# Kernel tuning notes

Measured on AMD Instinct MI355X. Metric: run time of the kernel, lower is better.

## Reference

```python
import jax, jax.numpy as jnp
import numpy as np

BS, NE, NN, CIN, H, D = 8, 4800, 4981, 3, 128, 6
EPG = 19200
NEDGE = BS * EPG
N = BS * NE

PARAM_NAMES = [
    'enc_cw1','enc_cb1','enc_cw2','enc_cb2','enc_cw3','enc_clng','enc_clnb',
    'enc_ew1','enc_eb1','enc_ew2','enc_eb2','enc_ew3','enc_elng','enc_elnb',
    'p_ew1','p_eb1','p_ew2','p_eb2','p_ew3','p_elng','p_elnb',
    'p_nw1','p_nb1','p_nw2','p_nb2','p_nw3','p_nlng','p_nlnb',
    'dec_uw1','dec_ub1','dec_uw2','dec_ub2','dec_uw3','dec_ulng','dec_ulnb',
    'dec_cw1','dec_cb1','dec_cw2','dec_cb2','dec_cw3']


def setup_inputs():
    key = jax.random.key(0)
    ks = iter(jax.random.split(key, 64))
    def nrm(shape, s=0.1):
        return jax.random.normal(next(ks), shape, jnp.float32) * s
    inp = {}
    inp['x'] = jax.random.normal(next(ks), (BS * NN, CIN), jnp.float32)
    inp['elem_conn'] = jax.random.randint(next(ks), (NE, 4), 0, NN)
    inp['edge_index'] = jax.random.randint(next(ks), (2, NEDGE), 0, N)
    inp['enc_cw1'] = nrm((CIN, 4, 1)); inp['enc_cb1'] = nrm((CIN, 1), 0.01)
    inp['enc_cw2'] = nrm((CIN, 1, 1)); inp['enc_cb2'] = nrm((CIN, 1), 0.01)
    inp['enc_cw3'] = nrm((CIN, 1, 1))
    inp['enc_clng'] = jnp.ones((CIN, 1)); inp['enc_clnb'] = jnp.zeros((CIN, 1))
    inp['enc_ew1'] = nrm((CIN, H)); inp['enc_eb1'] = nrm((H,), 0.01)
    inp['enc_ew2'] = nrm((H, H)); inp['enc_eb2'] = nrm((H,), 0.01)
    inp['enc_ew3'] = nrm((H, H))
    inp['enc_elng'] = jnp.ones((H,)); inp['enc_elnb'] = jnp.zeros((H,))
    inp['p_ew1'] = nrm((D, 2 * H, H)); inp['p_eb1'] = nrm((D, H), 0.01)
    inp['p_ew2'] = nrm((D, H, H)); inp['p_eb2'] = nrm((D, H), 0.01)
    inp['p_ew3'] = nrm((D, H, H))
    inp['p_elng'] = jnp.ones((D, H)); inp['p_elnb'] = jnp.zeros((D, H))
    inp['p_nw1'] = nrm((D, 2 * H, H)); inp['p_nb1'] = nrm((D, H), 0.01)
    inp['p_nw2'] = nrm((D, H, H)); inp['p_nb2'] = nrm((D, H), 0.01)
    inp['p_nw3'] = nrm((D, H, H))
    inp['p_nlng'] = jnp.ones((D, H)); inp['p_nlnb'] = jnp.zeros((D, H))
    inp['dec_uw1'] = nrm((H, 1, 4)); inp['dec_ub1'] = nrm((H, 4), 0.01)
    inp['dec_uw2'] = nrm((H, 4, 4)); inp['dec_ub2'] = nrm((H, 4), 0.01)
    inp['dec_uw3'] = nrm((H, 4, 4))
    inp['dec_ulng'] = jnp.ones((H, 4)); inp['dec_ulnb'] = jnp.zeros((H, 4))
    inp['dec_cw1'] = nrm((H, CIN)); inp['dec_cb1'] = nrm((CIN,), 0.01)
    inp['dec_cw2'] = nrm((CIN, CIN)); inp['dec_cb2'] = nrm((CIN,), 0.01)
    inp['dec_cw3'] = nrm((CIN, CIN))
    return inp


def lrelu(x):
    return jnp.where(x >= 0, x, 0.2 * x)


def ln(x, g, b, axis=-1):
    m = jnp.mean(x, axis=axis, keepdims=True)
    v = jnp.var(x, axis=axis, keepdims=True)
    return (x - m) / jnp.sqrt(v + 1e-5) * g + b


def mlp(x, w1, b1, w2, b2, w3):
    h = lrelu(x @ w1 + b1)
    h = lrelu(h @ w2 + b2)
    return h @ w3


def _forward(fl, elem_conn, edge_index):
    x = fl[0]
    P = dict(zip(PARAM_NAMES, fl[1:]))
    # ---- Encoder: MeshCNN gather (4 mesh nodes per element) + per-channel MLP 4->1 ----
    xg = x.reshape(BS, NN, CIN)[:, elem_conn]                  # (BS, NE, 4, CIN)
    h = lrelu(jnp.einsum('beic,cio->beoc', xg, P['enc_cw1']) + P['enc_cb1'].T[None, None])
    h = lrelu(jnp.einsum('beic,cio->beoc', h, P['enc_cw2']) + P['enc_cb2'].T[None, None])
    h = jnp.einsum('beic,cio->beoc', h, P['enc_cw3'])
    h = ln(h, P['enc_clng'].T[None, None], P['enc_clnb'].T[None, None], axis=2)  # LayerNorm(1)
    h = h[:, :, 0, :].reshape(N, CIN)
    h = ln(mlp(h, P['enc_ew1'], P['enc_eb1'], P['enc_ew2'], P['enc_eb2'], P['enc_ew3']),
           P['enc_elng'], P['enc_elnb'])                       # (N, H)
    # ---- Processor: D GraphNet blocks, edge MLP + scatter-add + node MLP ----
    src, dest = edge_index[0], edge_index[1]
    stacked = (P['p_ew1'], P['p_eb1'], P['p_ew2'], P['p_eb2'], P['p_ew3'], P['p_elng'], P['p_elnb'],
               P['p_nw1'], P['p_nb1'], P['p_nw2'], P['p_nb2'], P['p_nw3'], P['p_nlng'], P['p_nlnb'])
    def step(hc, p):
        ew1, eb1, ew2, eb2, ew3, eg, ebv, nw1, nb1, nw2, nb2, nw3, ng, nbv = p
        msg = jnp.concatenate([hc[dest], hc[src]], axis=-1)    # (NEDGE, 2H)
        m = ln(mlp(msg, ew1, eb1, ew2, eb2, ew3), eg, ebv)
        aggr = jax.ops.segment_sum(m, dest, num_segments=N)
        hn = ln(mlp(jnp.concatenate([hc, aggr], axis=-1), nw1, nb1, nw2, nb2, nw3), ng, nbv)
        return hn, None
    h, _ = jax.lax.scan(step, h, stacked)
    # ---- Decoder: per-channel upsample 1->4 then index_add back to mesh nodes ----
    u = h.reshape(BS, NE, H)[:, :, None, :]                    # (BS, NE, 1, H)
    u = lrelu(jnp.einsum('beic,cio->beoc', u, P['dec_uw1']) + P['dec_ub1'].T[None, None])
    u = lrelu(jnp.einsum('beic,cio->beoc', u, P['dec_uw2']) + P['dec_ub2'].T[None, None])
    u = jnp.einsum('beic,cio->beoc', u, P['dec_uw3'])
    u = ln(u, P['dec_ulng'].T[None, None], P['dec_ulnb'].T[None, None], axis=2)  # (BS, NE, 4, H)
    out = jnp.zeros((BS, NN, H), u.dtype).at[:, elem_conn.reshape(-1)].add(u.reshape(BS, NE * 4, H))
    out = out.reshape(BS * NN, H)
    o = lrelu(out @ P['dec_cw1'] + P['dec_cb1'])
    o = lrelu(o @ P['dec_cw2'] + P['dec_cb2'])
    return o @ P['dec_cw3']


def reference(x, elem_conn, edge_index,
              enc_cw1, enc_cb1, enc_cw2, enc_cb2, enc_cw3, enc_clng, enc_clnb,
              enc_ew1, enc_eb1, enc_ew2, enc_eb2, enc_ew3, enc_elng, enc_elnb,
              p_ew1, p_eb1, p_ew2, p_eb2, p_ew3, p_elng, p_elnb,
              p_nw1, p_nb1, p_nw2, p_nb2, p_nw3, p_nlng, p_nlnb,
              dec_uw1, dec_ub1, dec_uw2, dec_ub2, dec_uw3, dec_ulng, dec_ulnb,
              dec_cw1, dec_cb1, dec_cw2, dec_cb2, dec_cw3):
    fl = (x, enc_cw1, enc_cb1, enc_cw2, enc_cb2, enc_cw3, enc_clng, enc_clnb,
          enc_ew1, enc_eb1, enc_ew2, enc_eb2, enc_ew3, enc_elng, enc_elnb,
          p_ew1, p_eb1, p_ew2, p_eb2, p_ew3, p_elng, p_elnb,
          p_nw1, p_nb1, p_nw2, p_nb2, p_nw3, p_nlng, p_nlnb,
          dec_uw1, dec_ub1, dec_uw2, dec_ub2, dec_uw3, dec_ulng, dec_ulnb,
          dec_cw1, dec_cb1, dec_cw2, dec_cb2, dec_cw3)
    return _forward(fl, elem_conn, edge_index)
```

## Files before the change

### kernel.cpp

```cpp
#include <hip/hip_runtime.h>
#include <hip/hip_fp16.h>
#include <math.h>

#define BS    8
#define NE    4800
#define NN    4981
#define CIN   3
#define HD    128
#define DBLK  6
#define NEDGE 153600
#define NTOT  38400
#define NMESH (BS*NN)
#define NNP   5120
#define EM    128
#define NTILE (NEDGE / EM)
#define EGRID 240
#define TPB   (NTILE / EGRID)

#define UW1T  0
#define UB1T  512
#define UW2T  1024
#define UB2T  3072
#define UW3T  3584
#define ULNGT 5632
#define ULNBT 6144
#define DWT_N 6656

typedef _Float16 f16;
typedef _Float16 f16x8 __attribute__((ext_vector_type(8)));
typedef float f32x4 __attribute__((ext_vector_type(4)));

__device__ __forceinline__ float lrelu(float x) { return x >= 0.0f ? x : 0.2f * x; }

__global__ __launch_bounds__(128)
void enc_const_kernel(const float* __restrict__ clnb,
                      const float* __restrict__ ew1, const float* __restrict__ eb1,
                      const float* __restrict__ ew2, const float* __restrict__ eb2,
                      const float* __restrict__ ew3,
                      const float* __restrict__ g, const float* __restrict__ b,
                      float* __restrict__ hv0) {
    __shared__ float s1[HD], s2[HD], s3[HD];
    int j = threadIdx.x;
    float a = eb1[j];
    for (int c = 0; c < CIN; ++c) a += clnb[c] * ew1[c * HD + j];
    s1[j] = lrelu(a);
    __syncthreads();
    a = eb2[j];
    for (int k = 0; k < HD; ++k) a += s1[k] * ew2[k * HD + j];
    s2[j] = lrelu(a);
    __syncthreads();
    a = 0.0f;
    for (int k = 0; k < HD; ++k) a += s2[k] * ew3[k * HD + j];
    s3[j] = a;
    __syncthreads();
    float m = 0.0f;
    for (int k = 0; k < HD; ++k) m += s3[k];
    m *= (1.0f / HD);
    float v = 0.0f;
    for (int k = 0; k < HD; ++k) { float d = s3[k] - m; v += d * d; }
    v *= (1.0f / HD);
    float rs = 1.0f / sqrtf(v + 1e-5f);
    hv0[j] = (s3[j] - m) * rs * g[j] + b[j];
}

__global__ __launch_bounds__(128)
void msg0_kernel(const float* __restrict__ hv0,
                 const float* __restrict__ ew1, const float* __restrict__ eb1,
                 const float* __restrict__ ew2, const float* __restrict__ eb2,
                 const float* __restrict__ ew3,
                 const float* __restrict__ g, const float* __restrict__ b,
                 float* __restrict__ m0) {
    __shared__ float s1[HD], s2[HD], s3[HD];
    int j = threadIdx.x;
    float a = eb1[j];
    for (int k = 0; k < HD; ++k) a += hv0[k] * (ew1[k * HD + j] + ew1[(k + HD) * HD + j]);
    s1[j] = lrelu(a);
    __syncthreads();
    a = eb2[j];
    for (int k = 0; k < HD; ++k) a += s1[k] * ew2[k * HD + j];
    s2[j] = lrelu(a);
    __syncthreads();
    a = 0.0f;
    for (int k = 0; k < HD; ++k) a += s2[k] * ew3[k * HD + j];
    s3[j] = a;
    __syncthreads();
    float m = 0.0f;
    for (int k = 0; k < HD; ++k) m += s3[k];
    m *= (1.0f / HD);
    float v = 0.0f;
    for (int k = 0; k < HD; ++k) { float d = s3[k] - m; v += d * d; }
    v *= (1.0f / HD);
    float rs = 1.0f / sqrtf(v + 1e-5f);
    m0[j] = (s3[j] - m) * rs * g[j] + b[j];
}

__global__ __launch_bounds__(256)
void init_h16_kernel(f16* __restrict__ h, const float* __restrict__ hv0, int n8) {
    __shared__ f16 v[HD];
    if (threadIdx.x < HD) v[threadIdx.x] = (f16)hv0[threadIdx.x];
    __syncthreads();
    for (int i = blockIdx.x * blockDim.x + threadIdx.x; i < n8; i += gridDim.x * blockDim.x)
        ((uint4*)h)[i] = ((const uint4*)v)[i & 15];
}

__global__ __launch_bounds__(256)
void conv_weights_kernel(const float* __restrict__ ew1, const float* __restrict__ ew2,
                         const float* __restrict__ ew3,
                         const float* __restrict__ nw1, const float* __restrict__ nw2,
                         const float* __restrict__ nw3, f16* __restrict__ wbuf) {
    int b = blockIdx.x;
    int d = b >> 3, m = b & 7;
    const float* src;
    switch (m) {
        case 0: src = ew1 + (size_t)d * 2 * HD * HD; break;
        case 1: src = ew1 + (size_t)d * 2 * HD * HD + HD * HD; break;
        case 2: src = ew2 + (size_t)d * HD * HD; break;
        case 3: src = ew3 + (size_t)d * HD * HD; break;
        case 4: src = nw1 + (size_t)d * 2 * HD * HD; break;
        case 5: src = nw1 + (size_t)d * 2 * HD * HD + HD * HD; break;
        case 6: src = nw2 + (size_t)d * HD * HD; break;
        default: src = nw3 + (size_t)d * HD * HD; break;
    }
    f16* out = wbuf + (size_t)b * HD * HD;
    for (int idx = threadIdx.x; idx < HD * HD; idx += 256) {
        int n = idx >> 7, k = idx & 127;
        out[idx] = (f16)src[k * HD + n];
    }
}

__global__ __launch_bounds__(256)
void conv_ebias_kernel(const float* __restrict__ eb1, f16* __restrict__ eb16) {
    for (int i = threadIdx.x; i < DBLK * HD; i += 256)
        eb16[i] = (f16)eb1[i];
}

__global__ __launch_bounds__(256)
void conv_dec_weights(const float* __restrict__ uw1, const float* __restrict__ ub1,
                      const float* __restrict__ uw2, const float* __restrict__ ub2,
                      const float* __restrict__ uw3, const float* __restrict__ ulng,
                      const float* __restrict__ ulnb, float* __restrict__ dwt) {
    int tid = threadIdx.x;
    for (int idx = tid; idx < 512; idx += 256) {
        int o = idx >> 7, c = idx & 127;
        dwt[UW1T + idx] = uw1[c * 4 + o];
        dwt[UB1T + idx] = ub1[c * 4 + o];
        dwt[UB2T + idx] = ub2[c * 4 + o];
        dwt[ULNGT + idx] = ulng[c * 4 + o];
        dwt[ULNBT + idx] = ulnb[c * 4 + o];
    }
    for (int idx = tid; idx < 2048; idx += 256) {
        int io = idx >> 7, c = idx & 127;
        dwt[UW2T + idx] = uw2[c * 16 + io];
        dwt[UW3T + idx] = uw3[c * 16 + io];
    }
}

__global__ __launch_bounds__(256)
void csr_hist(const int* __restrict__ key, int* __restrict__ deg, int n) {
    int e = blockIdx.x * 256 + threadIdx.x;
    if (e < n) atomicAdd(&deg[key[e]], 1);
}

__global__ __launch_bounds__(256)
void csr_scan1(const int* __restrict__ deg, int* __restrict__ rowptr,
               int* __restrict__ bsum) {
    __shared__ int s[256];
    int i = blockIdx.x * 256 + threadIdx.x;
    int v = deg[i];
    s[threadIdx.x] = v;
    __syncthreads();
    for (int off = 1; off < 256; off <<= 1) {
        int t = (threadIdx.x >= off) ? s[threadIdx.x - off] : 0;
        __syncthreads();
        s[threadIdx.x] += t;
        __syncthreads();
    }
    rowptr[i] = s[threadIdx.x] - v;
    if (threadIdx.x == 255) bsum[blockIdx.x] = s[255];
}

__global__ __launch_bounds__(256)
void csr_scan2(int* __restrict__ bsum, int nb) {
    __shared__ int s[256];
    int v = (threadIdx.x < nb) ? bsum[threadIdx.x] : 0;
    s[threadIdx.x] = v;
    __syncthreads();
    for (int off = 1; off < 256; off <<= 1) {
        int t = (threadIdx.x >= off) ? s[threadIdx.x - off] : 0;
        __syncthreads();
        s[threadIdx.x] += t;
        __syncthreads();
    }
    if (threadIdx.x < nb) bsum[threadIdx.x] = s[threadIdx.x] - v;
}

__global__ __launch_bounds__(256)
void csr_scan3(int* __restrict__ rowptr, const int* __restrict__ bsum) {
    int i = blockIdx.x * 256 + threadIdx.x;
    rowptr[i] += bsum[blockIdx.x];
}

__global__ __launch_bounds__(256)
void csr_scatter(const int* __restrict__ dest, const int* __restrict__ srcv,
                 const int* __restrict__ rowptr, int* __restrict__ cursor,
                 int* __restrict__ dsorted, int* __restrict__ ssorted) {
    int e = blockIdx.x * 256 + threadIdx.x;
    int d = dest[e];
    int pos = rowptr[d] + atomicAdd(&cursor[d], 1);
    dsorted[pos] = d;
    ssorted[pos] = srcv[e];
}

__global__ __launch_bounds__(256)
void mesh_scatter(const int* __restrict__ conn, const int* __restrict__ mrow,
                  int* __restrict__ mcur, int* __restrict__ mslot, int n) {
    int idx = blockIdx.x * 256 + threadIdx.x;
    if (idx < n) {
        int nd = conn[idx];
        int pos = mrow[nd] + atomicAdd(&mcur[nd], 1);
        mslot[pos] = idx;
    }
}

template <int NT>
__device__ __forceinline__ void stage_w(const f16* __restrict__ Wg, f16 (*Bt)[HD + 8],
                                        int tid) {
    #pragma unroll
    for (int t = 0; t < 2048 / NT; ++t) {
        int idx = tid + t * NT;
        int r = idx >> 4, c = (idx & 15) * 8;
        *(uint4*)(&Bt[r][c]) = *(const uint4*)(Wg + (size_t)r * HD + c);
    }
}

__device__ __forceinline__ void mfma_pass(const f16 (*A)[HD + 8], const f16 (*Bt)[HD + 8],
                                          int rt_base, int ct_base, int ln, int quad,
                                          f32x4 acc[2][4]) {
    #pragma unroll
    for (int ks = 0; ks < 4; ++ks) {
        int kb = ks * 32 + quad * 8;
        f16x8 a0 = *(const f16x8*)(&A[rt_base + ln][kb]);
        f16x8 a1 = *(const f16x8*)(&A[rt_base + 16 + ln][kb]);
        #pragma unroll
        for (int c = 0; c < 4; ++c) {
            f16x8 b = *(const f16x8*)(&Bt[ct_base + c * 16 + ln][kb]);
            acc[0][c] = __builtin_amdgcn_mfma_f32_16x16x32_f16(a0, b, acc[0][c], 0, 0, 0);
            acc[1][c] = __builtin_amdgcn_mfma_f32_16x16x32_f16(a1, b, acc[1][c], 0, 0, 0);
        }
    }
}

__global__ __launch_bounds__(512, 2)
void gn_edge(const f16* __restrict__ P1, const f16* __restrict__ P2,
             const int* __restrict__ dsorted, const int* __restrict__ ssorted,
             const f16* __restrict__ W2, const f16* __restrict__ W3,
             const f16* __restrict__ b1h, const float* __restrict__ b2,
             const float* __restrict__ g, const float* __restrict__ bln,
             f16* __restrict__ msg) {
    __shared__ __align__(16) f16 Ag[2][EM][HD + 8];
    __shared__ __align__(16) f16 Bt2[HD][HD + 8];
    __shared__ __align__(16) f16 Bt3[HD][HD + 8];
    __shared__ float red[EM][2][2];

    const int tid = threadIdx.x;
    const int wave = tid >> 6, lane = tid & 63;
    const int ln = lane & 15, quad = lane >> 4;
    const int rt_base = (wave >> 1) * 32;
    const int ct_base = (wave & 1) * 64;
    const int half = wave & 1;
    const int r0 = tid >> 4;
    const int cg = (tid & 15) * 8;

    const int t0 = blockIdx.x * TPB;
    const int t1 = t0 + TPB;

    const f16 k02s = (f16)0.2f;
    const f16x8 k02 = {k02s, k02s, k02s, k02s, k02s, k02s, k02s, k02s};
    const f16x8 bb = *(const f16x8*)(b1h + cg);

    int dI[4], sI[4];
    #pragma unroll
    for (int it = 0; it < 4; ++it) {
        dI[it] = dsorted[t0 * EM + r0 + it * 32];
        sI[it] = ssorted[t0 * EM + r0 + it * 32];
    }
    stage_w<512>(W2, Bt2, tid);
    stage_w<512>(W3, Bt3, tid);
    #pragma unroll
    for (int it = 0; it < 4; ++it) {
        f16x8 p1 = *(const f16x8*)(P1 + (size_t)dI[it] * HD + cg);
        f16x8 p2 = *(const f16x8*)(P2 + (size_t)sI[it] * HD + cg);
        f16x8 s = p1 + p2 + bb;
        *(f16x8*)(&Ag[0][r0 + it * 32][cg]) = __builtin_elementwise_max(s, s * k02);
    }
    #pragma unroll
    for (int it = 0; it < 4; ++it) {
        dI[it] = dsorted[(t0 + 1) * EM + r0 + it * 32];
        sI[it] = ssorted[(t0 + 1) * EM + r0 + it * 32];
    }
    __syncthreads();

    int b = 0;
    for (int t = t0; t < t1; ++t, b ^= 1) {
        const int base = t * EM;
        f32x4 acc[2][4];

        #pragma unroll
        for (int c = 0; c < 4; ++c) {
            float bj = b2[ct_base + c * 16 + ln];
            f32x4 bv = {bj, bj, bj, bj};
            acc[0][c] = bv; acc[1][c] = bv;
        }
        mfma_pass(Ag[b], Bt2, rt_base, ct_base, ln, quad, acc);
        __syncthreads();

        const bool hasNext = (t + 1 < t1);
        f16x8 q1[4], q2[4];
        if (hasNext) {
            #pragma unroll
            for (int it = 0; it < 4; ++it) {
                q1[it] = *(const f16x8*)(P1 + (size_t)dI[it] * HD + cg);
                q2[it] = *(const f16x8*)(P2 + (size_t)sI[it] * HD + cg);
            }
        }
        #pragma unroll
        for (int i = 0; i < 2; ++i)
            #pragma unroll
            for (int c = 0; c < 4; ++c)
                #pragma unroll
                for (int r = 0; r < 4; ++r)
                    Ag[b][rt_base + i * 16 + quad * 4 + r][ct_base + c * 16 + ln] =
                        (f16)lrelu(acc[i][c][r]);
        if (t + 2 < t1) {
            #pragma unroll
            for (int it = 0; it < 4; ++it) {
                dI[it] = dsorted[(t + 2) * EM + r0 + it * 32];
                sI[it] = ssorted[(t + 2) * EM + r0 + it * 32];
            }
        }
        __syncthreads();

        #pragma unroll
        for (int c = 0; c < 4; ++c) { f32x4 z = {0,0,0,0}; acc[0][c] = z; acc[1][c] = z; }
        mfma_pass(Ag[b], Bt3, rt_base, ct_base, ln, quad, acc);

        #pragma unroll
        for (int i = 0; i < 2; ++i)
            #pragma unroll
            for (int r = 0; r < 4; ++r) {
                float s = acc[i][0][r] + acc[i][1][r] + acc[i][2][r] + acc[i][3][r];
                float q = acc[i][0][r] * acc[i][0][r] + acc[i][1][r] * acc[i][1][r] +
                          acc[i][2][r] * acc[i][2][r] + acc[i][3][r] * acc[i][3][r];
                s += __shfl_xor(s, 1); q += __shfl_xor(q, 1);
                s += __shfl_xor(s, 2); q += __shfl_xor(q, 2);
                s += __shfl_xor(s, 4); q += __shfl_xor(q, 4);
                s += __shfl_xor(s, 8); q += __shfl_xor(q, 8);
                if (ln == 0) {
                    int row = rt_base + i * 16 + quad * 4 + r;
                    red[row][half][0] = s;
                    red[row][half][1] = q;
                }
            }

        if (hasNext) {
            #pragma unroll
            for (int it = 0; it < 4; ++it) {
                f16x8 s = q1[it] + q2[it] + bb;
                *(f16x8*)(&Ag[b ^ 1][r0 + it * 32][cg]) =
                    __builtin_elementwise_max(s, s * k02);
            }
        }
        __syncthreads();

        float gv[4], bv[4];
        #pragma unroll
        for (int c = 0; c < 4; ++c) {
            int col = ct_base + c * 16 + ln;
            gv[c] = g[col]; bv[c] = bln[col];
        }
        #pragma unroll
        for (int i = 0; i < 2; ++i)
            #pragma unroll
            for (int r = 0; r < 4; ++r) {
                int row = rt_base + i * 16 + quad * 4 + r;
                float s = red[row][0][0] + red[row][1][0];
                float q = red[row][0][1] + red[row][1][1];
                float m = s * (1.0f / HD);
                float var = q * (1.0f / HD) - m * m;
                float rs = 1.0f / sqrtf(var + 1e-5f);
                #pragma unroll
                for (int c = 0; c < 4; ++c) {
                    int col = ct_base + c * 16 + ln;
                    float v = (acc[i][c][r] - m) * rs * gv[c] + bv[c];
                    msg[(size_t)(base + row) * HD + col] = (f16)v;
                }
            }
    }
}

template <int AGGR, bool PROD>
__global__ __launch_bounds__(256, 3)
void gn_node(f16* __restrict__ h16, const f16* __restrict__ msg,
             const int* __restrict__ rowptr, const int* __restrict__ deg,
             const float* __restrict__ m0,
             const f16* __restrict__ W1a, const f16* __restrict__ W1b,
             const f16* __restrict__ W2, const f16* __restrict__ W3,
             const float* __restrict__ b1, const float* __restrict__ b2,
             const float* __restrict__ g, const float* __restrict__ bln,
             const f16* __restrict__ nW1a, const f16* __restrict__ nW1b,
             f16* __restrict__ P1, f16* __restrict__ P2) {
    __shared__ __align__(16) f16 As[64][HD + 8];
    __shared__ __align__(16) f16 Bt[HD][HD + 8];
    __shared__ float red[64][2][2];
    int* rpS = (int*)&red[0][0][0];
    int* dgS = rpS + 64;

    const int tid = threadIdx.x;
    const int base = blockIdx.x * 64;
    const int wave = tid >> 6, lane = tid & 63;
    const int ln = lane & 15, quad = lane >> 4;
    const int rt_base = (wave >> 1) * 32;
    const int ct_base = (wave & 1) * 64;
    const int half = wave & 1;

    if (tid < 64) {
        if (AGGR == 1) rpS[tid] = rowptr[base + tid];
        dgS[tid] = deg[base + tid];
    }
    __syncthreads();

    f16x8 hreg[4];
    #pragma unroll
    for (int t = 0; t < 4; ++t) {
        int idx = tid + t * 256;
        int r = idx >> 4, c = (idx & 15) * 8;
        hreg[t] = *(const f16x8*)(h16 + (size_t)(base + r) * HD + c);
        if (AGGR == 0) {
            float sc = (float)dgS[r];
            f16x8 o;
            #pragma unroll
            for (int u = 0; u < 8; ++u) o[u] = (f16)(sc * m0[c + u]);
            *(f16x8*)(&As[r][c]) = o;
        } else {
            int rp = rpS[r], dg = dgS[r];
            float a[8] = {0, 0, 0, 0, 0, 0, 0, 0};
            for (int j = 0; j < dg; ++j) {
                f16x8 mv = *(const f16x8*)(msg + (size_t)(rp + j) * HD + c);
                #pragma unroll
                for (int u = 0; u < 8; ++u) a[u] += (float)mv[u];
            }
            f16x8 o;
            #pragma unroll
            for (int u = 0; u < 8; ++u) o[u] = (f16)a[u];
            *(f16x8*)(&As[r][c]) = o;
        }
    }
    stage_w<256>(W1b, Bt, tid);
    __syncthreads();

    f32x4 acc[2][4];
    #pragma unroll
    for (int c = 0; c < 4; ++c) {
        float bj = b1[ct_base + c * 16 + ln];
        f32x4 bb = {bj, bj, bj, bj};
        acc[0][c] = bb; acc[1][c] = bb;
    }
    mfma_pass(As, Bt, rt_base, ct_base, ln, quad, acc);
    __syncthreads();

    #pragma unroll
    for (int t = 0; t < 4; ++t) {
        int idx = tid + t * 256;
        int r = idx >> 4, c = (idx & 15) * 8;
        *(f16x8*)(&As[r][c]) = hreg[t];
    }
    stage_w<256>(W1a, Bt, tid);
    __syncthreads();
    mfma_pass(As, Bt, rt_base, ct_base, ln, quad, acc);
    __syncthreads();

    stage_w<256>(W2, Bt, tid);
    #pragma unroll
    for (int i = 0; i < 2; ++i)
        #pragma unroll
        for (int c = 0; c < 4; ++c)
            #pragma unroll
            for (int r = 0; r < 4; ++r)
                As[rt_base + i * 16 + quad * 4 + r][ct_base + c * 16 + ln] =
                    (f16)lrelu(acc[i][c][r]);
    __syncthreads();

    #pragma unroll
    for (int c = 0; c < 4; ++c) {
        float bj = b2[ct_base + c * 16 + ln];
        f32x4 bb = {bj, bj, bj, bj};
        acc[0][c] = bb; acc[1][c] = bb;
    }
    mfma_pass(As, Bt, rt_base, ct_base, ln, quad, acc);
    __syncthreads();
    stage_w<256>(W3, Bt, tid);
    #pragma unroll
    for (int i = 0; i < 2; ++i)
        #pragma unroll
        for (int c = 0; c < 4; ++c)
            #pragma unroll
            for (int r = 0; r < 4; ++r)
                As[rt_base + i * 16 + quad * 4 + r][ct_base + c * 16 + ln] =
                    (f16)lrelu(acc[i][c][r]);
    __syncthreads();

    #pragma unroll
    for (int c = 0; c < 4; ++c) { f32x4 z = {0,0,0,0}; acc[0][c] = z; acc[1][c] = z; }
    mfma_pass(As, Bt, rt_base, ct_base, ln, quad, acc);

    #pragma unroll
    for (int i = 0; i < 2; ++i)
        #pragma unroll
        for (int r = 0; r < 4; ++r) {
            float s = acc[i][0][r] + acc[i][1][r] + acc[i][2][r] + acc[i][3][r];
            float q = acc[i][0][r] * acc[i][0][r] + acc[i][1][r] * acc[i][1][r] +
                      acc[i][2][r] * acc[i][2][r] + acc[i][3][r] * acc[i][3][r];
            s += __shfl_xor(s, 1); q += __shfl_xor(q, 1);
            s += __shfl_xor(s, 2); q += __shfl_xor(q, 2);
            s += __shfl_xor(s, 4); q += __shfl_xor(q, 4);
            s += __shfl_xor(s, 8); q += __shfl_xor(q, 8);
            if (ln == 0) {
                int row = rt_base + i * 16 + quad * 4 + r;
                red[row][half][0] = s;
                red[row][half][1] = q;
            }
        }
    __syncthreads();

    float gv[4], bv[4];
    #pragma unroll
    for (int c = 0; c < 4; ++c) {
        int col = ct_base + c * 16 + ln;
        gv[c] = g[col]; bv[c] = bln[col];
    }
    #pragma unroll
    for (int i = 0; i < 2; ++i)
        #pragma unroll
        for (int r = 0; r < 4; ++r) {
            int row = rt_base + i * 16 + quad * 4 + r;
            float s = red[row][0][0] + red[row][1][0];
            float q = red[row][0][1] + red[row][1][1];
            float m = s * (1.0f / HD);
            float var = q * (1.0f / HD) - m * m;
            float rs = 1.0f / sqrtf(var + 1e-5f);
            #pragma unroll
            for (int c = 0; c < 4; ++c) {
                int col = ct_base + c * 16 + ln;
                float v = (acc[i][c][r] - m) * rs * gv[c] + bv[c];
                f16 hv = (f16)v;
                h16[(size_t)(base + row) * HD + col] = hv;
                if (PROD) As[row][col] = hv;
            }
        }

    if (PROD) {
        __syncthreads();
        stage_w<256>(nW1a, Bt, tid);
        __syncthreads();
        #pragma unroll
        for (int c = 0; c < 4; ++c) { f32x4 z = {0,0,0,0}; acc[0][c] = z; acc[1][c] = z; }
        mfma_pass(As, Bt, rt_base, ct_base, ln, quad, acc);
        #pragma unroll
        for (int i = 0; i < 2; ++i)
            #pragma unroll
            for (int c = 0; c < 4; ++c)
                #pragma unroll
                for (int r = 0; r < 4; ++r)
                    P1[(size_t)(base + rt_base + i * 16 + quad * 4 + r) * HD +
                       ct_base + c * 16 + ln] = (f16)acc[i][c][r];
        __syncthreads();
        stage_w<256>(nW1b, Bt, tid);
        __syncthreads();
        #pragma unroll
        for (int c = 0; c < 4; ++c) { f32x4 z = {0,0,0,0}; acc[0][c] = z; acc[1][c] = z; }
        mfma_pass(As, Bt, rt_base, ct_base, ln, quad, acc);
        #pragma unroll
        for (int i = 0; i < 2; ++i)
            #pragma unroll
            for (int c = 0; c < 4; ++c)
                #pragma unroll
                for (int r = 0; r < 4; ++r)
                    P2[(size_t)(base + rt_base + i * 16 + quad * 4 + r) * HD +
                       ct_base + c * 16 + ln] = (f16)acc[i][c][r];
    }
}

__global__ __launch_bounds__(256)
void dec_store_kernel(const f16* __restrict__ h, const float* __restrict__ dwt,
                      f16* __restrict__ uval) {
    __shared__ f16 ub[2][4][HD];
    int tid = threadIdx.x;
    int idx = blockIdx.x * 256 + tid;
    int c = idx & 127;
    int nl = tid >> 7;
    float s = (float)h[idx];
    float u1[4], u2[4], u3[4];
    #pragma unroll
    for (int o = 0; o < 4; ++o)
        u1[o] = lrelu(s * dwt[UW1T + o * 128 + c] + dwt[UB1T + o * 128 + c]);
    #pragma unroll
    for (int o = 0; o < 4; ++o) {
        float a = dwt[UB2T + o * 128 + c];
        #pragma unroll
        for (int i = 0; i < 4; ++i) a += u1[i] * dwt[UW2T + (i * 4 + o) * 128 + c];
        u2[o] = lrelu(a);
    }
    #pragma unroll
    for (int o = 0; o < 4; ++o) {
        float a = 0.f;
        #pragma unroll
        for (int i = 0; i < 4; ++i) a += u2[i] * dwt[UW3T + (i * 4 + o) * 128 + c];
        u3[o] = a;
    }
    float m = 0.25f * (u3[0] + u3[1] + u3[2] + u3[3]);
    float var = 0.f;
    #pragma unroll
    for (int o = 0; o < 4; ++o) { float d = u3[o] - m; var += d * d; }
    var *= 0.25f;
    float rs = 1.0f / sqrtf(var + 1e-5f);
    #pragma unroll
    for (int o = 0; o < 4; ++o) {
        float val = (u3[o] - m) * rs * dwt[ULNGT + o * 128 + c] + dwt[ULNBT + o * 128 + c];
        ub[nl][o][c] = (f16)val;
    }
    __syncthreads();
    int nl2 = tid >> 7, rem = tid & 127;
    uint2 v = ((const uint2*)&ub[nl2][0][0])[rem];
    ((uint2*)(uval + (size_t)(blockIdx.x * 2 + nl2) * 4 * HD))[rem] = v;
}

__global__ __launch_bounds__(256)
void dec_gather_out(const f16* __restrict__ uval,
                    const int* __restrict__ mrow, const int* __restrict__ mdeg,
                    const int* __restrict__ mslot,
                    const float* __restrict__ cw1, const float* __restrict__ cb1,
                    const float* __restrict__ cw2, const float* __restrict__ cb2,
                    const float* __restrict__ cw3,
                    float* __restrict__ o, int nrows) {
    int r = blockIdx.x * 4 + (threadIdx.x >> 6);
    if (r >= nrows) return;
    int lane = threadIdx.x & 63;
    int b = r / NN, n = r - b * NN;
    int rp = mrow[n], dg = mdeg[n];
    size_t boff = (size_t)b * NE * 4;
    float a0 = 0.f, a1 = 0.f;
    for (int j = 0; j < dg; ++j) {
        int slot = mslot[rp + j];
        const f16* up = uval + (boff + slot) * HD + lane * 2;
        a0 += (float)up[0];
        a1 += (float)up[1];
    }
    int c0 = lane * 2, c1 = lane * 2 + 1;
    float s[3];
    #pragma unroll
    for (int k = 0; k < 3; ++k)
        s[k] = a0 * cw1[c0 * 3 + k] + a1 * cw1[c1 * 3 + k];
    #pragma unroll
    for (int off = 32; off >= 1; off >>= 1) {
        s[0] += __shfl_down(s[0], off);
        s[1] += __shfl_down(s[1], off);
        s[2] += __shfl_down(s[2], off);
    }
    if (lane == 0) {
        float t1[3], t2[3];
        #pragma unroll
        for (int k = 0; k < 3; ++k) t1[k] = lrelu(s[k] + cb1[k]);
        #pragma unroll
        for (int k = 0; k < 3; ++k) {
            float a = cb2[k];
            #pragma unroll
            for (int q = 0; q < 3; ++q) a += t1[q] * cw2[q * 3 + k];
            t2[k] = lrelu(a);
        }
        #pragma unroll
        for (int k = 0; k < 3; ++k) {
            float a = 0.f;
            #pragma unroll
            for (int q = 0; q < 3; ++q) a += t2[q] * cw3[q * 3 + k];
            o[(size_t)r * 3 + k] = a;
        }
    }
}

extern "C" void kernel_launch(void* const* d_in, const int* in_sizes, int n_in,
                              void* d_out, int out_size, void* d_ws, size_t ws_size,
                              hipStream_t stream) {
    const int* elem_conn = (const int*)d_in[1];
    const int* edge_index = (const int*)d_in[2];
    const int* e_src = edge_index;
    const int* e_dst = edge_index + NEDGE;
    const float* enc_clnb = (const float*)d_in[9];
    const float* enc_ew1 = (const float*)d_in[10];
    const float* enc_eb1 = (const float*)d_in[11];
    const float* enc_ew2 = (const float*)d_in[12];
    const float* enc_eb2 = (const float*)d_in[13];
    const float* enc_ew3 = (const float*)d_in[14];
    const float* enc_elng = (const float*)d_in[15];
    const float* enc_elnb = (const float*)d_in[16];
    const float* p_ew1 = (const float*)d_in[17];
    const float* p_eb1 = (const float*)d_in[18];
    const float* p_ew2 = (const float*)d_in[19];
    const float* p_eb2 = (const float*)d_in[20];
    const float* p_ew3 = (const float*)d_in[21];
    const float* p_elng = (const float*)d_in[22];
    const float* p_elnb = (const float*)d_in[23];
    const float* p_nw1 = (const float*)d_in[24];
    const float* p_nb1 = (const float*)d_in[25];
    const float* p_nw2 = (const float*)d_in[26];
    const float* p_nb2 = (const float*)d_in[27];
    const float* p_nw3 = (const float*)d_in[28];
    const float* p_nlng = (const float*)d_in[29];
    const float* p_nlnb = (const float*)d_in[30];
    const float* dec_uw1 = (const float*)d_in[31];
    const float* dec_ub1 = (const float*)d_in[32];
    const float* dec_uw2 = (const float*)d_in[33];
    const float* dec_ub2 = (const float*)d_in[34];
    const float* dec_uw3 = (const float*)d_in[35];
    const float* dec_ulng = (const float*)d_in[36];
    const float* dec_ulnb = (const float*)d_in[37];
    const float* dec_cw1 = (const float*)d_in[38];
    const float* dec_cb1 = (const float*)d_in[39];
    const float* dec_cw2 = (const float*)d_in[40];
    const float* dec_cb2 = (const float*)d_in[41];
    const float* dec_cw3 = (const float*)d_in[42];

    char* ws = (char*)d_ws;
    f16*   h16     = (f16*)(ws);
    f16*   wbuf    = (f16*)(ws + 9830400);
    float* hv0     = (float*)(ws + 11403264);
    float* m0      = (float*)(ws + 11403776);
    f16*   P1      = (f16*)(ws + 11404288);
    f16*   P2      = (f16*)(ws + 21234688);
    f16*   msg     = (f16*)(ws + 31065088);
    f16*   uval    = (f16*)(ws + 31065088);
    int*   deg     = (int*)(ws + 70386688);
    int*   rowptr  = (int*)(ws + 70540288);
    int*   cursor  = (int*)(ws + 70693888);
    int*   bsum    = (int*)(ws + 70847488);
    int*   dsorted = (int*)(ws + 70848512);
    int*   ssorted = (int*)(ws + 71462912);
    int*   mdeg    = (int*)(ws + 70693888);
    int*   mrow    = (int*)(ws + 70714368);
    int*   mcur    = (int*)(ws + 70734848);
    int*   mbsum   = (int*)(ws + 70755328);
    int*   mslot   = (int*)(ws + 70756352);
    float* dwt     = (float*)P1;
    f16*   eb16    = (f16*)(ws + 72077312);

    enc_const_kernel<<<1, 128, 0, stream>>>(enc_clnb, enc_ew1, enc_eb1, enc_ew2,
                                            enc_eb2, enc_ew3, enc_elng, enc_elnb, hv0);
    init_h16_kernel<<<1200, 256, 0, stream>>>(h16, hv0, NTOT * HD / 8);
    conv_weights_kernel<<<48, 256, 0, stream>>>(p_ew1, p_ew2, p_ew3,
                                                p_nw1, p_nw2, p_nw3, wbuf);
    conv_ebias_kernel<<<1, 256, 0, stream>>>(p_eb1, eb16);
    msg0_kernel<<<1, 128, 0, stream>>>(hv0, p_ew1, p_eb1, p_ew2, p_eb2, p_ew3,
                                       p_elng, p_elnb, m0);

    hipMemsetAsync(deg, 0, NTOT * sizeof(int), stream);
    hipMemsetAsync(cursor, 0, NTOT * sizeof(int), stream);
    csr_hist<<<NEDGE / 256, 256, 0, stream>>>(e_dst, deg, NEDGE);
    csr_scan1<<<NTOT / 256, 256, 0, stream>>>(deg, rowptr, bsum);
    csr_scan2<<<1, 256, 0, stream>>>(bsum, NTOT / 256);
    csr_scan3<<<NTOT / 256, 256, 0, stream>>>(rowptr, bsum);
    csr_scatter<<<NEDGE / 256, 256, 0, stream>>>(e_dst, e_src, rowptr, cursor,
                                                 dsorted, ssorted);

    hipMemsetAsync(mdeg, 0, NNP * sizeof(int), stream);
    hipMemsetAsync(mcur, 0, NNP * sizeof(int), stream);
    csr_hist<<<(NE * 4 + 255) / 256, 256, 0, stream>>>(elem_conn, mdeg, NE * 4);
    csr_scan1<<<NNP / 256, 256, 0, stream>>>(mdeg, mrow, mbsum);
    csr_scan2<<<1, 256, 0, stream>>>(mbsum, NNP / 256);
    csr_scan3<<<NNP / 256, 256, 0, stream>>>(mrow, mbsum);
    mesh_scatter<<<(NE * 4 + 255) / 256, 256, 0, stream>>>(elem_conn, mrow, mcur,
                                                           mslot, NE * 4);

    {
        const f16* wd = wbuf;
        const f16* wn = wbuf + (size_t)8 * HD * HD;
        gn_node<0, true><<<NTOT / 64, 256, 0, stream>>>(
            h16, nullptr, nullptr, deg, m0,
            wd + 4 * HD * HD, wd + 5 * HD * HD, wd + 6 * HD * HD, wd + 7 * HD * HD,
            p_nb1, p_nb2, p_nlng, p_nlnb,
            wn + 0 * HD * HD, wn + 1 * HD * HD, P1, P2);
    }

    for (int d = 1; d < DBLK; ++d) {
        const f16* wd = wbuf + (size_t)d * 8 * HD * HD;
        gn_edge<<<EGRID, 512, 0, stream>>>(
            P1, P2, dsorted, ssorted,
            wd + 2 * HD * HD, wd + 3 * HD * HD,
            eb16 + (size_t)d * HD, p_eb2 + (size_t)d * HD,
            p_elng + (size_t)d * HD, p_elnb + (size_t)d * HD, msg);
        if (d < DBLK - 1) {
            const f16* wn = wbuf + (size_t)(d + 1) * 8 * HD * HD;
            gn_node<1, true><<<NTOT / 64, 256, 0, stream>>>(
                h16, msg, rowptr, deg, nullptr,
                wd + 4 * HD * HD, wd + 5 * HD * HD, wd + 6 * HD * HD, wd + 7 * HD * HD,
                p_nb1 + (size_t)d * HD, p_nb2 + (size_t)d * HD,
                p_nlng + (size_t)d * HD, p_nlnb + (size_t)d * HD,
                wn + 0 * HD * HD, wn + 1 * HD * HD, P1, P2);
        } else {
            gn_node<1, false><<<NTOT / 64, 256, 0, stream>>>(
                h16, msg, rowptr, deg, nullptr,
                wd + 4 * HD * HD, wd + 5 * HD * HD, wd + 6 * HD * HD, wd + 7 * HD * HD,
                p_nb1 + (size_t)d * HD, p_nb2 + (size_t)d * HD,
                p_nlng + (size_t)d * HD, p_nlnb + (size_t)d * HD,
                wbuf, wbuf, P1, P2);
        }
    }

    conv_dec_weights<<<1, 256, 0, stream>>>(dec_uw1, dec_ub1, dec_uw2, dec_ub2,
                                            dec_uw3, dec_ulng, dec_ulnb, dwt);
    dec_store_kernel<<<NTOT * HD / 256, 256, 0, stream>>>(h16, dwt, uval);
    dec_gather_out<<<(NMESH + 3) / 4, 256, 0, stream>>>(
        uval, mrow, mdeg, mslot, dec_cw1, dec_cb1, dec_cw2, dec_cb2, dec_cw3,
        (float*)d_out, NMESH);
}
```

Measured before the change: 655.2 us.

## Enlarge gn_node tiles to 128 rows with 512 threads and prefetch next weights

Each gn_node block now covers 128 node rows with 8 waves instead of 64 rows with 4, so every staged weight matrix is reused across twice as many rows. The next block's W1a/W1b weights are loaded into registers early and written to shared memory later, which removes one barrier-separated staging step. The message aggregation loop is unrolled by four so more independent loads are in flight. In exchange, shared memory per block and register pressure go up, fewer blocks can run at once, and the larger tiles may leave some CUs idle at the tail.

Result: slower. 686.5 us (+4.8%).

```diff
diff --git a/kernel.cpp b/kernel.cpp
--- a/kernel.cpp
+++ b/kernel.cpp
@@ -399,7 +399,7 @@
 }
 
 template <int AGGR, bool PROD>
-__global__ __launch_bounds__(256, 3)
+__global__ __launch_bounds__(512, 4)
 void gn_node(f16* __restrict__ h16, const f16* __restrict__ msg,
              const int* __restrict__ rowptr, const int* __restrict__ deg,
              const float* __restrict__ m0,
@@ -409,21 +409,21 @@
              const float* __restrict__ g, const float* __restrict__ bln,
              const f16* __restrict__ nW1a, const f16* __restrict__ nW1b,
              f16* __restrict__ P1, f16* __restrict__ P2) {
-    __shared__ __align__(16) f16 As[64][HD + 8];
+    __shared__ __align__(16) f16 As[EM][HD + 8];
     __shared__ __align__(16) f16 Bt[HD][HD + 8];
-    __shared__ float red[64][2][2];
+    __shared__ float red[EM][2][2];
     int* rpS = (int*)&red[0][0][0];
-    int* dgS = rpS + 64;
+    int* dgS = rpS + EM;
 
     const int tid = threadIdx.x;
-    const int base = blockIdx.x * 64;
+    const int base = blockIdx.x * EM;
     const int wave = tid >> 6, lane = tid & 63;
     const int ln = lane & 15, quad = lane >> 4;
     const int rt_base = (wave >> 1) * 32;
     const int ct_base = (wave & 1) * 64;
     const int half = wave & 1;
 
-    if (tid < 64) {
+    if (tid < EM) {
         if (AGGR == 1) rpS[tid] = rowptr[base + tid];
         dgS[tid] = deg[base + tid];
     }
@@ -432,7 +432,7 @@
     f16x8 hreg[4];
     #pragma unroll
     for (int t = 0; t < 4; ++t) {
-        int idx = tid + t * 256;
+        int idx = tid + t * 512;
         int r = idx >> 4, c = (idx & 15) * 8;
         hreg[t] = *(const f16x8*)(h16 + (size_t)(base + r) * HD + c);
         if (AGGR == 0) {
@@ -444,7 +444,17 @@
         } else {
             int rp = rpS[r], dg = dgS[r];
             float a[8] = {0, 0, 0, 0, 0, 0, 0, 0};
-            for (int j = 0; j < dg; ++j) {
+            int j = 0;
+            for (; j + 4 <= dg; j += 4) {
+                f16x8 v0 = *(const f16x8*)(msg + (size_t)(rp + j) * HD + c);
+                f16x8 v1 = *(const f16x8*)(msg + (size_t)(rp + j + 1) * HD + c);
+                f16x8 v2 = *(const f16x8*)(msg + (size_t)(rp + j + 2) * HD + c);
+                f16x8 v3 = *(const f16x8*)(msg + (size_t)(rp + j + 3) * HD + c);
+                #pragma unroll
+                for (int u = 0; u < 8; ++u)
+                    a[u] += ((float)v0[u] + (float)v1[u]) + ((float)v2[u] + (float)v3[u]);
+            }
+            for (; j < dg; ++j) {
                 f16x8 mv = *(const f16x8*)(msg + (size_t)(rp + j) * HD + c);
                 #pragma unroll
                 for (int u = 0; u < 8; ++u) a[u] += (float)mv[u];
@@ -455,7 +465,7 @@
             *(f16x8*)(&As[r][c]) = o;
         }
     }
-    stage_w<256>(W1b, Bt, tid);
+    stage_w<512>(W1b, Bt, tid);
     __syncthreads();
 
     f32x4 acc[2][4];
@@ -470,16 +480,16 @@
 
     #pragma unroll
     for (int t = 0; t < 4; ++t) {
-        int idx = tid + t * 256;
+        int idx = tid + t * 512;
         int r = idx >> 4, c = (idx & 15) * 8;
         *(f16x8*)(&As[r][c]) = hreg[t];
     }
-    stage_w<256>(W1a, Bt, tid);
+    stage_w<512>(W1a, Bt, tid);
     __syncthreads();
     mfma_pass(As, Bt, rt_base, ct_base, ln, quad, acc);
     __syncthreads();
 
-    stage_w<256>(W2, Bt, tid);
+    stage_w<512>(W2, Bt, tid);
     #pragma unroll
     for (int i = 0; i < 2; ++i)
         #pragma unroll
@@ -498,7 +508,7 @@
     }
     mfma_pass(As, Bt, rt_base, ct_base, ln, quad, acc);
     __syncthreads();
-    stage_w<256>(W3, Bt, tid);
+    stage_w<512>(W3, Bt, tid);
     #pragma unroll
     for (int i = 0; i < 2; ++i)
         #pragma unroll
@@ -512,6 +522,16 @@
     #pragma unroll
     for (int c = 0; c < 4; ++c) { f32x4 z = {0,0,0,0}; acc[0][c] = z; acc[1][c] = z; }
     mfma_pass(As, Bt, rt_base, ct_base, ln, quad, acc);
+
+    uint4 wr[4];
+    if (PROD) {
+        #pragma unroll
+        for (int t = 0; t < 4; ++t) {
+            int idx = tid + t * 512;
+            int r = idx >> 4, c = (idx & 15) * 8;
+            wr[t] = *(const uint4*)(nW1a + (size_t)r * HD + c);
+        }
+    }
 
     #pragma unroll
     for (int i = 0; i < 2; ++i)
@@ -532,6 +552,15 @@
         }
     __syncthreads();
 
+    if (PROD) {
+        #pragma unroll
+        for (int t = 0; t < 4; ++t) {
+            int idx = tid + t * 512;
+            int r = idx >> 4, c = (idx & 15) * 8;
+            *(uint4*)(&Bt[r][c]) = wr[t];
+        }
+    }
+
     float gv[4], bv[4];
     #pragma unroll
     for (int c = 0; c < 4; ++c) {
@@ -560,8 +589,12 @@
 
     if (PROD) {
         __syncthreads();
-        stage_w<256>(nW1a, Bt, tid);
-        __syncthreads();
+        #pragma unroll
+        for (int t = 0; t < 4; ++t) {
+            int idx = tid + t * 512;
+            int r = idx >> 4, c = (idx & 15) * 8;
+            wr[t] = *(const uint4*)(nW1b + (size_t)r * HD + c);
+        }
         #pragma unroll
         for (int c = 0; c < 4; ++c) { f32x4 z = {0,0,0,0}; acc[0][c] = z; acc[1][c] = z; }
         mfma_pass(As, Bt, rt_base, ct_base, ln, quad, acc);
@@ -574,7 +607,12 @@
                     P1[(size_t)(base + rt_base + i * 16 + quad * 4 + r) * HD +
                        ct_base + c * 16 + ln] = (f16)acc[i][c][r];
         __syncthreads();
-        stage_w<256>(nW1b, Bt, tid);
+        #pragma unroll
+        for (int t = 0; t < 4; ++t) {
+            int idx = tid + t * 512;
+            int r = idx >> 4, c = (idx & 15) * 8;
+            *(uint4*)(&Bt[r][c]) = wr[t];
+        }
         __syncthreads();
         #pragma unroll
         for (int c = 0; c < 4; ++c) { f32x4 z = {0,0,0,0}; acc[0][c] = z; acc[1][c] = z; }
@@ -782,7 +820,7 @@
     {
         const f16* wd = wbuf;
         const f16* wn = wbuf + (size_t)8 * HD * HD;
-        gn_node<0, true><<<NTOT / 64, 256, 0, stream>>>(
+        gn_node<0, true><<<NTOT / EM, 512, 0, stream>>>(
             h16, nullptr, nullptr, deg, m0,
             wd + 4 * HD * HD, wd + 5 * HD * HD, wd + 6 * HD * HD, wd + 7 * HD * HD,
             p_nb1, p_nb2, p_nlng, p_nlnb,
@@ -798,14 +836,14 @@
             p_elng + (size_t)d * HD, p_elnb + (size_t)d * HD, msg);
         if (d < DBLK - 1) {
             const f16* wn = wbuf + (size_t)(d + 1) * 8 * HD * HD;
-            gn_node<1, true><<<NTOT / 64, 256, 0, stream>>>(
+            gn_node<1, true><<<NTOT / EM, 512, 0, stream>>>(
                 h16, msg, rowptr, deg, nullptr,
                 wd + 4 * HD * HD, wd + 5 * HD * HD, wd + 6 * HD * HD, wd + 7 * HD * HD,
                 p_nb1 + (size_t)d * HD, p_nb2 + (size_t)d * HD,
                 p_nlng + (size_t)d * HD, p_nlnb + (size_t)d * HD,
                 wn + 0 * HD * HD, wn + 1 * HD * HD, P1, P2);
         } else {
-            gn_node<1, false><<<NTOT / 64, 256, 0, stream>>>(
+            gn_node<1, false><<<NTOT / EM, 512, 0, stream>>>(
                 h16, msg, rowptr, deg, nullptr,
                 wd + 4 * HD * HD, wd + 5 * HD * HD, wd + 6 * HD * HD, wd + 7 * HD * HD,
                 p_nb1 + (size_t)d * HD, p_nb2 + (size_t)d * HD,
```
